# Kernel optimization log

Hardware: AMD Instinct MI355X
Metric: run time of the kernel (lower is better)

The kernel has to match this reference:

```python
import jax, jax.numpy as jnp
import numpy as np

EMBED = 768
HEADS = 12
HEAD_DIM = EMBED // HEADS
DEPTH = 4
PATCH = 16
GRID = 32  # 512 / 16
MLP_DIM = 4 * EMBED
LN_EPS = 1e-5


def layer_norm(x, w, b):
    m = jnp.mean(x, axis=-1, keepdims=True)
    v = jnp.mean(jnp.square(x - m), axis=-1, keepdims=True)
    return (x - m) * jax.lax.rsqrt(v + LN_EPS) * w + b


def sam_attention(x, qkv_w, qkv_b, proj_w, proj_b, rel_pos_h, rel_pos_w):
    B, H, W, C = x.shape
    N = H * W
    scale = HEAD_DIM ** -0.5
    qkv = x.reshape(B, N, C) @ qkv_w + qkv_b  # (B, N, 3C)
    qkv = qkv.reshape(B, N, 3, HEADS, HEAD_DIM).transpose(2, 0, 3, 1, 4)
    qkv = qkv.reshape(3, B * HEADS, N, HEAD_DIM)
    q, k, v = qkv[0], qkv[1], qkv[2]
    attn = jnp.einsum('bqc,bkc->bqk', q * scale, k)  # (B*nh, N, N)
    # decomposed relative position (q_size == k_size, table already max_rel_dist)
    idx_h = jnp.arange(H)[:, None] - jnp.arange(H)[None, :] + (H - 1)
    idx_w = jnp.arange(W)[:, None] - jnp.arange(W)[None, :] + (W - 1)
    Rh = rel_pos_h[idx_h]  # (H, H, hd)
    Rw = rel_pos_w[idx_w]  # (W, W, hd)
    r_q = q.reshape(B * HEADS, H, W, HEAD_DIM)
    rel_h = jnp.einsum('bhwc,hkc->bhwk', r_q, Rh)
    rel_w = jnp.einsum('bhwc,wkc->bhwk', r_q, Rw)
    attn = (attn.reshape(B * HEADS, H, W, H, W)
            + rel_h[:, :, :, :, None]
            + rel_w[:, :, :, None, :]).reshape(B * HEADS, N, N)
    attn = jax.nn.softmax(attn, axis=-1)
    out = (attn @ v).reshape(B, HEADS, H, W, HEAD_DIM)
    out = out.transpose(0, 2, 3, 1, 4).reshape(B, H, W, C)
    return out @ proj_w + proj_b


def setup_inputs() -> dict:
    key = jax.random.key(0)
    ks = jax.random.split(key, 20)
    s = lambda k, shape, sc=0.02: jax.random.normal(k, shape, jnp.float32) * sc
    inp = {
        'x': jax.random.normal(ks[0], (4, 3, 512, 512), jnp.float32),
        'conv_w': s(ks[1], (EMBED, 3, PATCH, PATCH)),
        'conv_b': jnp.zeros((EMBED,), jnp.float32),
        'pos_embed': s(ks[2], (1, GRID, GRID, EMBED)),
        'ln1_w': jnp.ones((DEPTH, EMBED), jnp.float32),
        'ln1_b': jnp.zeros((DEPTH, EMBED), jnp.float32),
        'qkv_w': s(ks[3], (DEPTH, EMBED, 3 * EMBED)),
        'qkv_b': jnp.zeros((DEPTH, 3 * EMBED), jnp.float32),
        'proj_w': s(ks[4], (DEPTH, EMBED, EMBED)),
        'proj_b': jnp.zeros((DEPTH, EMBED), jnp.float32),
        'rel_pos_h': s(ks[5], (DEPTH, 2 * GRID - 1, HEAD_DIM)),
        'rel_pos_w': s(ks[6], (DEPTH, 2 * GRID - 1, HEAD_DIM)),
        'ln2_w': jnp.ones((DEPTH, EMBED), jnp.float32),
        'ln2_b': jnp.zeros((DEPTH, EMBED), jnp.float32),
        'fc1_w': s(ks[7], (DEPTH, EMBED, MLP_DIM)),
        'fc1_b': jnp.zeros((DEPTH, MLP_DIM), jnp.float32),
        'fc2_w': s(ks[8], (DEPTH, MLP_DIM, EMBED)),
        'fc2_b': jnp.zeros((DEPTH, EMBED), jnp.float32),
    }
    return inp


def reference(x, conv_w, conv_b, pos_embed, ln1_w, ln1_b, qkv_w, qkv_b,
              proj_w, proj_b, rel_pos_h, rel_pos_w, ln2_w, ln2_b,
              fc1_w, fc1_b, fc2_w, fc2_b):
    # patch embed: conv stride=patch, then NCHW -> NHWC
    h = jax.lax.conv_general_dilated(
        x, conv_w, window_strides=(PATCH, PATCH), padding='VALID',
        dimension_numbers=('NCHW', 'OIHW', 'NCHW'))
    h = h.transpose(0, 2, 3, 1) + conv_b  # (B, 32, 32, 768)
    h = h + pos_embed
    for i in range(DEPTH):
        a = sam_attention(layer_norm(h, ln1_w[i], ln1_b[i]),
                          qkv_w[i], qkv_b[i], proj_w[i], proj_b[i],
                          rel_pos_h[i], rel_pos_w[i])
        h = h + a
        m = layer_norm(h, ln2_w[i], ln2_b[i])
        m = jax.nn.gelu(m @ fc1_w[i] + fc1_b[i], approximate=False) @ fc2_w[i] + fc2_b[i]
        h = h + m
    return h
```

## Files before the change

kernel.cpp:

```cpp
#include <hip/hip_runtime.h>
#include <hip/hip_bf16.h>
#include <math.h>
#include <stdint.h>

#define EMBED 768
#define NTOK  1024
#define BATCH 4
#define NHEAD 12
#define HD    64
#define MLPD  3072
#define M_ROWS 4096

typedef __attribute__((ext_vector_type(8))) short short8;
typedef __attribute__((ext_vector_type(4))) float floatx4;

__device__ __forceinline__ float b2f(__hip_bfloat16 v) { return __bfloat162float(v); }

__device__ __forceinline__ void gld_lds16(const void* g, void* l) {
    __builtin_amdgcn_global_load_lds(
        (const __attribute__((address_space(1))) uint32_t*)g,
        (__attribute__((address_space(3))) uint32_t*)l, 16, 0, 0);
}

__device__ __forceinline__ int swz(int row, int c) { return row*64 + (((c) ^ (row & 7)) << 3); }

__device__ __forceinline__ void xcd_remap(int gx, int gy, int& bx, int& by) {
    int id  = blockIdx.x + gx*blockIdx.y;
    int nwg = gx*gy;
    int q = nwg >> 3, r = nwg & 7;
    int xcd = id & 7, idx = id >> 3;
    int nid = (xcd < r ? xcd*(q+1) : r*(q+1) + (xcd-r)*q) + idx;
    bx = nid % gx;
    by = nid / gx;
}

__global__ __launch_bounds__(256)
void im2col(const float* __restrict__ x, __hip_bfloat16* __restrict__ A)
{
    int p  = blockIdx.x;
    int b  = p >> 10;
    int n  = p & 1023;
    int gh = n >> 5, gw = n & 31;
    int tid = threadIdx.x;
    for (int i = tid; i < 768; i += 256) {
        int ci = i >> 8, r = i & 255, kh = r >> 4, kw = r & 15;
        A[(size_t)p*768 + i] = __float2bfloat16(
            x[(((size_t)b*3 + ci)*512 + (gh*16 + kh))*512 + gw*16 + kw]);
    }
}

__global__ __launch_bounds__(256)
void cvt_bf16(const float* __restrict__ in, __hip_bfloat16* __restrict__ out, int n)
{
    int i = blockIdx.x*256 + threadIdx.x;
    if (i < n) out[i] = __float2bfloat16(in[i]);
}

__global__ __launch_bounds__(256)
void layernorm_bf16(const float* __restrict__ in,
                    const float* __restrict__ w,
                    const float* __restrict__ b,
                    __hip_bfloat16* __restrict__ out)
{
    int row = blockIdx.x;
    const float* xr = in + (size_t)row*768;
    int tid = threadIdx.x;
    float v0 = xr[tid], v1 = xr[tid+256], v2 = xr[tid+512];
    float s = v0+v1+v2, ss = v0*v0+v1*v1+v2*v2;
    __shared__ float rs[256], rss[256];
    rs[tid] = s; rss[tid] = ss; __syncthreads();
    for (int o = 128; o > 0; o >>= 1) {
        if (tid < o) { rs[tid] += rs[tid+o]; rss[tid] += rss[tid+o]; }
        __syncthreads();
    }
    float mean = rs[0] * (1.f/768.f);
    float var  = rss[0] * (1.f/768.f) - mean*mean;
    float inv  = rsqrtf(var + 1e-5f);
    out[(size_t)row*768 + tid]     = __float2bfloat16((v0-mean)*inv*w[tid]     + b[tid]);
    out[(size_t)row*768 + tid+256] = __float2bfloat16((v1-mean)*inv*w[tid+256] + b[tid+256]);
    out[(size_t)row*768 + tid+512] = __float2bfloat16((v2-mean)*inv*w[tid+512] + b[tid+512]);
}

__global__ __launch_bounds__(256)
void resum_ln(float* __restrict__ h,
              const float* __restrict__ p0, const float* __restrict__ p1,
              const float* __restrict__ bias,
              const float* __restrict__ w, const float* __restrict__ b,
              __hip_bfloat16* __restrict__ out)
{
    int row = blockIdx.x;
    int tid = threadIdx.x;
    size_t base = (size_t)row*768;
    float v[3];
    float s = 0.f, ss = 0.f;
    #pragma unroll
    for (int e = 0; e < 3; ++e) {
        int i = tid + e*256;
        float val = h[base+i] + p0[base+i] + p1[base+i] + bias[i];
        h[base+i] = val;
        v[e] = val; s += val; ss += val*val;
    }
    __shared__ float rs[256], rss[256];
    rs[tid] = s; rss[tid] = ss; __syncthreads();
    for (int o = 128; o > 0; o >>= 1) {
        if (tid < o) { rs[tid] += rs[tid+o]; rss[tid] += rss[tid+o]; }
        __syncthreads();
    }
    float mean = rs[0] * (1.f/768.f);
    float var  = rss[0] * (1.f/768.f) - mean*mean;
    float inv  = rsqrtf(var + 1e-5f);
    #pragma unroll
    for (int e = 0; e < 3; ++e) {
        int i = tid + e*256;
        out[base+i] = __float2bfloat16((v[e]-mean)*inv*w[i] + b[i]);
    }
}

__global__ __launch_bounds__(256)
void resum_out(const float* __restrict__ h,
               const float* __restrict__ p0, const float* __restrict__ p1,
               const float* __restrict__ bias,
               float* __restrict__ out)
{
    int i = blockIdx.x*256 + threadIdx.x;
    out[i] = h[i] + p0[i] + p1[i] + bias[i % 768];
}

__global__ __launch_bounds__(256)
void prep_weights(const float* __restrict__ qkv_w,  const float* __restrict__ proj_w,
                  const float* __restrict__ fc1_w,  const float* __restrict__ fc2_w,
                  __hip_bfloat16* __restrict__ qkv_wt, __hip_bfloat16* __restrict__ proj_wt,
                  __hip_bfloat16* __restrict__ fc1_wt, __hip_bfloat16* __restrict__ fc2_wt)
{
    int id = blockIdx.x;
    const float* src; __hip_bfloat16* dst; int K, N, bx, by;
    if (id < 1728)      {            src = qkv_w;  dst = qkv_wt;  K = 768;  N = 2304; bx = id % 72; by = id / 72; }
    else if (id < 2304) { id -= 1728; src = proj_w; dst = proj_wt; K = 768;  N = 768;  bx = id % 24; by = id / 24; }
    else if (id < 4608) { id -= 2304; src = fc1_w;  dst = fc1_wt;  K = 768;  N = 3072; bx = id % 96; by = id / 96; }
    else                { id -= 4608; src = fc2_w;  dst = fc2_wt;  K = 3072; N = 768;  bx = id % 24; by = id / 24; }

    __shared__ float t[32][33];
    int n0 = bx*32, k0 = by*32;
    int tx = threadIdx.x & 31, ty = threadIdx.x >> 5;
    #pragma unroll
    for (int r = 0; r < 4; ++r) {
        int row = ty + r*8;
        t[row][tx] = src[(size_t)(k0+row)*N + n0 + tx];
    }
    __syncthreads();
    #pragma unroll
    for (int r = 0; r < 4; ++r) {
        int row = ty + r*8;
        dst[(size_t)(n0+row)*K + k0 + tx] = __float2bfloat16(t[tx][row]);
    }
}

__global__ __launch_bounds__(256)
void gemm64(const __hip_bfloat16* __restrict__ A,
            const __hip_bfloat16* __restrict__ Bt,
            const float* __restrict__ bias,
            const float* __restrict__ res,
            const float* __restrict__ posadd,
            float* __restrict__ Cf,
            int M, int N, int K)
{
    __shared__ __align__(16) char smem[24576];

    const int tid  = threadIdx.x;
    const int lane = tid & 63;
    const int wid  = tid >> 6;
    const int wr   = wid >> 1;
    const int wc   = wid & 1;
    const int lr   = lane & 15;
    const int quad = lane >> 4;

    int bx, by;
    xcd_remap(gridDim.x, gridDim.y, bx, by);
    const int bm = by * 64;
    const int bn = bx * 128;

    const int srow  = tid >> 2;
    const int skoff = (tid & 3) * 8;
    const int wbase = wid * 1024;

    floatx4 acc[2][4];
    #pragma unroll
    for (int i = 0; i < 2; ++i)
        #pragma unroll
        for (int j = 0; j < 4; ++j)
            acc[i][j] = (floatx4){0.f,0.f,0.f,0.f};

    auto stage = [&](int bq, int k0) {
        char* base = smem + bq*12288 + wbase;
        gld_lds16(A + (size_t)(bm + srow)*K + k0 + skoff, base);
        #pragma unroll
        for (int c = 0; c < 2; ++c)
            gld_lds16(Bt + (size_t)(bn + c*64 + srow)*K + k0 + skoff,
                      base + 4096 + c*4096);
    };

    const int nt = K >> 5;
    stage(0, 0);
    __syncthreads();
    int cur = 0;
    for (int t = 0; t < nt; ++t) {
        if (t + 1 < nt) stage(cur ^ 1, (t+1)*32);

        const __hip_bfloat16* As = (const __hip_bfloat16*)(smem + cur*12288);
        const __hip_bfloat16* Bs = As + 2048;

        short8 a[2], b[4];
        #pragma unroll
        for (int i = 0; i < 2; ++i)
            a[i] = *(const short8*)((const void*)(As + (wr*32 + i*16 + lr)*32 + quad*8));
        #pragma unroll
        for (int j = 0; j < 4; ++j)
            b[j] = *(const short8*)((const void*)(Bs + (wc*64 + j*16 + lr)*32 + quad*8));
        #pragma unroll
        for (int i = 0; i < 2; ++i)
            #pragma unroll
            for (int j = 0; j < 4; ++j)
                acc[i][j] = __builtin_amdgcn_mfma_f32_16x16x32_bf16(a[i], b[j], acc[i][j], 0, 0, 0);
        __syncthreads();
        cur ^= 1;
    }

    #pragma unroll
    for (int j = 0; j < 4; ++j) {
        int col = bn + wc*64 + j*16 + lr;
        float bs = bias[col];
        #pragma unroll
        for (int i = 0; i < 2; ++i) {
            #pragma unroll
            for (int r = 0; r < 4; ++r) {
                int row = bm + wr*32 + i*16 + quad*4 + r;
                float val = acc[i][j][r] + bs;
                if (res)    val += res[(size_t)row*N + col];
                if (posadd) val += posadd[(size_t)(row & 1023)*N + col];
                Cf[(size_t)row*N + col] = val;
            }
        }
    }
}

__global__ __launch_bounds__(256)
void gemm128(const __hip_bfloat16* __restrict__ A,
             const __hip_bfloat16* __restrict__ Bt,
             const float* __restrict__ bias,
             float* __restrict__ Cf,
             __hip_bfloat16* __restrict__ Cb,
             __hip_bfloat16* __restrict__ qp,
             __hip_bfloat16* __restrict__ kp,
             __hip_bfloat16* __restrict__ vp,
             int M, int N, int K, int S, int dogelu, int emode)
{
    __shared__ __align__(16) char smem[32768];

    const int tid  = threadIdx.x;
    const int lane = tid & 63;
    const int wid  = tid >> 6;
    const int wr   = wid >> 1;
    const int wc   = wid & 1;
    const int lr   = lane & 15;
    const int quad = lane >> 4;

    int bx, by;
    xcd_remap(gridDim.x, gridDim.y, bx, by);
    const int bm = by * 128;
    const int bn = bx * 128;
    const int z  = blockIdx.z;
    const int Kseg = K / S;
    const int kbeg = z * Kseg;

    const int srow  = tid >> 2;
    const int skoff = (tid & 3) * 8;
    const int wbase = wid * 1024;

    floatx4 acc[4][4];
    #pragma unroll
    for (int i = 0; i < 4; ++i)
        #pragma unroll
        for (int j = 0; j < 4; ++j)
            acc[i][j] = (floatx4){0.f,0.f,0.f,0.f};

    auto stage = [&](int bq, int k0) {
        char* base = smem + bq*16384 + wbase;
        #pragma unroll
        for (int c = 0; c < 2; ++c)
            gld_lds16(A + (size_t)(bm + c*64 + srow)*K + k0 + skoff,
                      base + c*4096);
        #pragma unroll
        for (int c = 0; c < 2; ++c)
            gld_lds16(Bt + (size_t)(bn + c*64 + srow)*K + k0 + skoff,
                      base + 8192 + c*4096);
    };

    const int nt = Kseg >> 5;
    stage(0, kbeg);
    __syncthreads();
    int cur = 0;
    for (int t = 0; t < nt; ++t) {
        if (t + 1 < nt) stage(cur ^ 1, kbeg + (t+1)*32);

        const __hip_bfloat16* As = (const __hip_bfloat16*)(smem + cur*16384);
        const __hip_bfloat16* Bs = As + 4096;

        short8 a[4], b[4];
        #pragma unroll
        for (int i = 0; i < 4; ++i)
            a[i] = *(const short8*)((const void*)(As + (wr*64 + i*16 + lr)*32 + quad*8));
        #pragma unroll
        for (int j = 0; j < 4; ++j)
            b[j] = *(const short8*)((const void*)(Bs + (wc*64 + j*16 + lr)*32 + quad*8));
        #pragma unroll
        for (int i = 0; i < 4; ++i)
            #pragma unroll
            for (int j = 0; j < 4; ++j)
                acc[i][j] = __builtin_amdgcn_mfma_f32_16x16x32_bf16(a[i], b[j], acc[i][j], 0, 0, 0);
        __syncthreads();
        cur ^= 1;
    }

    if (emode == 3) {
        #pragma unroll
        for (int j = 0; j < 4; ++j) {
            int col = bn + wc*64 + j*16 + lr;
            #pragma unroll
            for (int i = 0; i < 4; ++i) {
                #pragma unroll
                for (int r = 0; r < 4; ++r) {
                    int row = bm + wr*64 + i*16 + quad*4 + r;
                    Cf[(size_t)z*M*N + (size_t)row*N + col] = acc[i][j][r];
                }
            }
        }
        return;
    }

    __hip_bfloat16* epi = (__hip_bfloat16*)(smem + wid*4864);

    if (emode == 1) {
        #pragma unroll
        for (int p = 0; p < 2; ++p) {
            #pragma unroll
            for (int j = 0; j < 4; ++j) {
                float bs = bias[bn + wc*64 + j*16 + lr];
                #pragma unroll
                for (int ii = 0; ii < 2; ++ii) {
                    int i = p*2 + ii;
                    #pragma unroll
                    for (int r = 0; r < 4; ++r) {
                        float val = acc[i][j][r] + bs;
                        if (dogelu) val = 0.5f*val*(1.f + erff(val*0.70710678118f));
                        epi[(ii*16 + quad*4 + r)*72 + j*16 + lr] = __float2bfloat16(val);
                    }
                }
            }
            #pragma unroll
            for (int p2 = 0; p2 < 4; ++p2) {
                int row = p2*8 + (lane >> 3), chunk = lane & 7;
                short8 v = *(const short8*)((const void*)(epi + row*72 + chunk*8));
                *(short8*)((void*)(Cb + (size_t)(bm + wr*64 + p*32 + row)*N
                                      + bn + wc*64 + chunk*8)) = v;
            }
        }
        return;
    }

    const int head64 = (bn + wc*64) >> 6;
    const int which  = head64 / 12;
    const int head   = head64 % 12;
    const int b_     = (bm + wr*64) >> 10;
    const int bh     = b_*NHEAD + head;
    const int n0     = (bm + wr*64) & 1023;

    if (which < 2) {
        __hip_bfloat16* dst = (which == 0 ? qp : kp) + ((size_t)bh*NTOK + n0)*HD;
        #pragma unroll
        for (int p = 0; p < 2; ++p) {
            #pragma unroll
            for (int j = 0; j < 4; ++j) {
                float bs = bias[bn + wc*64 + j*16 + lr];
                #pragma unroll
                for (int ii = 0; ii < 2; ++ii) {
                    int i = p*2 + ii;
                    #pragma unroll
                    for (int r = 0; r < 4; ++r)
                        epi[(ii*16 + quad*4 + r)*72 + j*16 + lr] =
                            __float2bfloat16(acc[i][j][r] + bs);
                }
            }
            #pragma unroll
            for (int p2 = 0; p2 < 4; ++p2) {
                int row = p2*8 + (lane >> 3), chunk = lane & 7;
                short8 v = *(const short8*)((const void*)(epi + row*72 + chunk*8));
                *(short8*)((void*)(dst + (size_t)(p*32 + row)*HD + chunk*8)) = v;
            }
        }
    } else {
        __hip_bfloat16* dstv = vp + (size_t)bh*HD*NTOK + n0;
        #pragma unroll
        for (int p = 0; p < 2; ++p) {
            #pragma unroll
            for (int j = 0; j < 4; ++j) {
                float bs = bias[bn + wc*64 + j*16 + lr];
                #pragma unroll
                for (int ii = 0; ii < 2; ++ii) {
                    int i = p*2 + ii;
                    #pragma unroll
                    for (int r = 0; r < 4; ++r)
                        epi[(j*16 + lr)*36 + ii*16 + quad*4 + r] =
                            __float2bfloat16(acc[i][j][r] + bs);
                }
            }
            #pragma unroll
            for (int p2 = 0; p2 < 4; ++p2) {
                int d = p2*16 + (lane >> 2), chunk = lane & 3;
                short8 v = *(const short8*)((const void*)(epi + d*36 + chunk*8));
                *(short8*)((void*)(dstv + (size_t)d*NTOK + p*32 + chunk*8)) = v;
            }
        }
    }
}

__global__ __launch_bounds__(256)
void attention_mfma(const __hip_bfloat16* __restrict__ qp,
                    const __hip_bfloat16* __restrict__ kp,
                    const __hip_bfloat16* __restrict__ vp,
                    const float* __restrict__ rph,
                    const float* __restrict__ rpw,
                    __hip_bfloat16* __restrict__ out)
{
    const int blk  = blockIdx.x;
    const int bh   = blk >> 4;
    const int qt   = blk & 15;
    const int b    = bh / NHEAD;
    const int head = bh % NHEAD;
    const int tid  = threadIdx.x;
    const int lane = tid & 63;
    const int w    = tid >> 6;
    const int lr   = lane & 15;
    const int quad = lane >> 4;

    __shared__ __align__(16) __hip_bfloat16 Qs[64*64];
    __shared__ __align__(16) __hip_bfloat16 Ks[64*64];
    __shared__ __align__(16) __hip_bfloat16 Vs[64*64];
    __shared__ __align__(16) __hip_bfloat16 Ps[4*16*64];
    __shared__ float relhS[64*32];
    __shared__ float relwS[64*32];

    const __hip_bfloat16* qb = qp + ((size_t)bh*NTOK + qt*64)*HD;
    const __hip_bfloat16* kb = kp + (size_t)bh*NTOK*HD;
    const __hip_bfloat16* vb = vp + (size_t)bh*HD*NTOK;

    const int sr = tid >> 2;
    const int sc = (tid & 3) * 2;

    short8 kreg0, kreg1, vreg0, vreg1;
    {
        const __hip_bfloat16* kk = kb + (size_t)sr*HD + sc*8;
        kreg0 = *(const short8*)((const void*)kk);
        kreg1 = *(const short8*)((const void*)(kk + 8));
        const __hip_bfloat16* vv = vb + (size_t)sr*NTOK + sc*8;
        vreg0 = *(const short8*)((const void*)vv);
        vreg1 = *(const short8*)((const void*)(vv + 8));
    }

    {
        const __hip_bfloat16* qq = qb + (size_t)sr*HD + sc*8;
        short8 q0 = *(const short8*)((const void*)qq);
        short8 q1 = *(const short8*)((const void*)(qq + 8));
        *(short8*)((void*)(Qs + swz(sr, sc)))   = q0;
        *(short8*)((void*)(Qs + swz(sr, sc+1))) = q1;
    }

    for (int i = tid; i < 504; i += 256) {
        int r = i >> 3, c = i & 7;
        const float* ph = rph + (size_t)r*HD + c*8;
        const float* pw = rpw + (size_t)r*HD + c*8;
        union { short8 v; __hip_bfloat16 e[8]; } uh, uw;
        #pragma unroll
        for (int e = 0; e < 8; ++e) { uh.e[e] = __float2bfloat16(ph[e]); uw.e[e] = __float2bfloat16(pw[e]); }
        *(short8*)((void*)(Ks + swz(r, c))) = uh.v;
        *(short8*)((void*)(Vs + swz(r, c))) = uw.v;
    }
    if (tid < 16) {
        short8 z = (short8){0,0,0,0,0,0,0,0};
        int c = tid & 7;
        if (tid < 8) *(short8*)((void*)(Ks + swz(63, c))) = z;
        else         *(short8*)((void*)(Vs + swz(63, c))) = z;
    }
    __syncthreads();

    short8 qa0 = *(const short8*)((const void*)(Qs + swz(w*16 + lr, quad)));
    short8 qa1 = *(const short8*)((const void*)(Qs + swz(w*16 + lr, 4 + quad)));

    const int qrow = w*16 + quad*4;
    const int qh_  = qt*2 + (w >> 1);
    const int qw_  = (w & 1)*16 + quad*4;

    #pragma unroll
    for (int j = 0; j < 4; ++j) {
        int t = j*16 + lr;
        short8 th0 = *(const short8*)((const void*)(Ks + swz(j*16 + lr, quad)));
        short8 th1 = *(const short8*)((const void*)(Ks + swz(j*16 + lr, 4 + quad)));
        floatx4 ha = (floatx4){0.f,0.f,0.f,0.f};
        ha = __builtin_amdgcn_mfma_f32_16x16x32_bf16(qa0, th0, ha, 0, 0, 0);
        ha = __builtin_amdgcn_mfma_f32_16x16x32_bf16(qa1, th1, ha, 0, 0, 0);
        short8 tw0 = *(const short8*)((const void*)(Vs + swz(j*16 + lr, quad)));
        short8 tw1 = *(const short8*)((const void*)(Vs + swz(j*16 + lr, 4 + quad)));
        floatx4 wa = (floatx4){0.f,0.f,0.f,0.f};
        wa = __builtin_amdgcn_mfma_f32_16x16x32_bf16(qa0, tw0, wa, 0, 0, 0);
        wa = __builtin_amdgcn_mfma_f32_16x16x32_bf16(qa1, tw1, wa, 0, 0, 0);
        int kh = qh_ + 31 - t;
        #pragma unroll
        for (int rr = 0; rr < 4; ++rr) {
            if (kh >= 0 && kh < 32) relhS[(qrow + rr)*32 + kh] = ha[rr];
            int kw = qw_ + rr + 31 - t;
            if (kw >= 0 && kw < 32) relwS[(qrow + rr)*32 + kw] = wa[rr];
        }
    }

    float rw[4][2];
    #pragma unroll
    for (int rr = 0; rr < 4; ++rr)
        #pragma unroll
        for (int jp = 0; jp < 2; ++jp)
            rw[rr][jp] = relwS[(qrow + rr)*32 + jp*16 + lr];

    floatx4 o[4];
    #pragma unroll
    for (int ds = 0; ds < 4; ++ds) o[ds] = (floatx4){0.f,0.f,0.f,0.f};
    float lsum[4] = {0.f, 0.f, 0.f, 0.f};

    const float scale = 0.125f;

    for (int kt = 0; kt < 16; ++kt) {
        __syncthreads();
        *(short8*)((void*)(Ks + swz(sr, sc)))   = kreg0;
        *(short8*)((void*)(Ks + swz(sr, sc+1))) = kreg1;
        *(short8*)((void*)(Vs + swz(sr, sc)))   = vreg0;
        *(short8*)((void*)(Vs + swz(sr, sc+1))) = vreg1;
        __syncthreads();

        if (kt < 15) {
            const __hip_bfloat16* kk = kb + (size_t)(kt+1)*64*HD + (size_t)sr*HD + sc*8;
            kreg0 = *(const short8*)((const void*)kk);
            kreg1 = *(const short8*)((const void*)(kk + 8));
            const __hip_bfloat16* vv = vb + (size_t)sr*NTOK + (kt+1)*64 + sc*8;
            vreg0 = *(const short8*)((const void*)vv);
            vreg1 = *(const short8*)((const void*)(vv + 8));
        }

        float2 rh2[4];
        #pragma unroll
        for (int rr = 0; rr < 4; ++rr)
            rh2[rr] = *(const float2*)((const void*)(relhS + (qrow + rr)*32 + kt*2));

        floatx4 sv[4];
        #pragma unroll
        for (int j = 0; j < 4; ++j) {
            short8 kb0 = *(const short8*)((const void*)(Ks + swz(j*16 + lr, quad)));
            short8 kb1 = *(const short8*)((const void*)(Ks + swz(j*16 + lr, 4 + quad)));
            floatx4 z = (floatx4){0.f,0.f,0.f,0.f};
            z = __builtin_amdgcn_mfma_f32_16x16x32_bf16(qa0, kb0, z, 0, 0, 0);
            z = __builtin_amdgcn_mfma_f32_16x16x32_bf16(qa1, kb1, z, 0, 0, 0);
            sv[j] = z;
        }

        #pragma unroll
        for (int j = 0; j < 4; ++j) {
            int colc = j*2 + (lr >> 3);
            #pragma unroll
            for (int rr = 0; rr < 4; ++rr) {
                float s = sv[j][rr]*scale + ((j < 2) ? rh2[rr].x : rh2[rr].y) + rw[rr][j & 1];
                s = fminf(fmaxf(s, -60.f), 60.f);
                float pp = __expf(s);
                lsum[rr] += pp;
                int prow = quad*4 + rr;
                Ps[w*1024 + prow*64 + ((colc ^ (prow & 7)) << 3) + (lr & 7)] = __float2bfloat16(pp);
            }
        }

        short8 pa0 = *(const short8*)((const void*)(Ps + w*1024 + swz(lr, quad)));
        short8 pa1 = *(const short8*)((const void*)(Ps + w*1024 + swz(lr, 4 + quad)));
        #pragma unroll
        for (int ds = 0; ds < 4; ++ds) {
            short8 v0 = *(const short8*)((const void*)(Vs + swz(ds*16 + lr, quad)));
            short8 v1 = *(const short8*)((const void*)(Vs + swz(ds*16 + lr, 4 + quad)));
            o[ds] = __builtin_amdgcn_mfma_f32_16x16x32_bf16(pa0, v0, o[ds], 0, 0, 0);
            o[ds] = __builtin_amdgcn_mfma_f32_16x16x32_bf16(pa1, v1, o[ds], 0, 0, 0);
        }
    }

    #pragma unroll
    for (int off = 1; off < 16; off <<= 1)
        #pragma unroll
        for (int rr = 0; rr < 4; ++rr)
            lsum[rr] += __shfl_xor(lsum[rr], off, 16);

    #pragma unroll
    for (int rr = 0; rr < 4; ++rr) {
        float inv = 1.f / lsum[rr];
        int n = qt*64 + w*16 + quad*4 + rr;
        size_t base = ((size_t)b*NTOK + n)*EMBED + head*HD;
        #pragma unroll
        for (int ds = 0; ds < 4; ++ds)
            out[base + ds*16 + lr] = __float2bfloat16(o[ds][rr] * inv);
    }
}

extern "C" void kernel_launch(void* const* d_in, const int* in_sizes, int n_in,
                              void* d_out, int out_size, void* d_ws, size_t ws_size,
                              hipStream_t stream)
{
    const float* x      = (const float*)d_in[0];
    const float* conv_w = (const float*)d_in[1];
    const float* conv_b = (const float*)d_in[2];
    const float* pos    = (const float*)d_in[3];
    const float* ln1_w  = (const float*)d_in[4];
    const float* ln1_b  = (const float*)d_in[5];
    const float* qkv_w  = (const float*)d_in[6];
    const float* qkv_b  = (const float*)d_in[7];
    const float* proj_w = (const float*)d_in[8];
    const float* proj_b = (const float*)d_in[9];
    const float* rph    = (const float*)d_in[10];
    const float* rpw    = (const float*)d_in[11];
    const float* ln2_w  = (const float*)d_in[12];
    const float* ln2_b  = (const float*)d_in[13];
    const float* fc1_w  = (const float*)d_in[14];
    const float* fc1_b  = (const float*)d_in[15];
    const float* fc2_w  = (const float*)d_in[16];
    const float* fc2_b  = (const float*)d_in[17];

    char* p = (char*)d_ws;
    float*           h       = (float*)p;           p += (size_t)M_ROWS*EMBED*4;
    __hip_bfloat16*  q_perm  = (__hip_bfloat16*)p;
    float*           p0      = (float*)p;           p += (size_t)48*NTOK*HD*2;
    __hip_bfloat16*  k_perm  = (__hip_bfloat16*)p;  p += (size_t)48*NTOK*HD*2;
    __hip_bfloat16*  vt_perm = (__hip_bfloat16*)p;  p += (size_t)48*NTOK*HD*2;
    __hip_bfloat16*  attn_o  = (__hip_bfloat16*)p;  p += (size_t)M_ROWS*EMBED*2;
    __hip_bfloat16*  x_ln    = (__hip_bfloat16*)p;  p += (size_t)M_ROWS*EMBED*2;
    __hip_bfloat16*  mlp     = (__hip_bfloat16*)p;  p += (size_t)M_ROWS*MLPD*2;
    __hip_bfloat16*  qkv_wt  = (__hip_bfloat16*)p;  p += (size_t)2304*768*2;
    __hip_bfloat16*  proj_wt = (__hip_bfloat16*)p;  p += (size_t)768*768*2;
    __hip_bfloat16*  fc1_wt  = (__hip_bfloat16*)p;  p += (size_t)MLPD*768*2;
    __hip_bfloat16*  fc2_wt  = (__hip_bfloat16*)p;  p += (size_t)768*MLPD*2;

    __hip_bfloat16*  A_im    = mlp;
    __hip_bfloat16*  conv_wt = qkv_wt;

    im2col<<<M_ROWS, 256, 0, stream>>>(x, A_im);
    cvt_bf16<<<(768*768 + 255)/256, 256, 0, stream>>>(conv_w, conv_wt, 768*768);
    gemm64<<<dim3(768/128, M_ROWS/64, 1), 256, 0, stream>>>(
        A_im, conv_wt, conv_b, nullptr, pos, h, M_ROWS, 768, 768);

    layernorm_bf16<<<M_ROWS, 256, 0, stream>>>(h, ln1_w, ln1_b, x_ln);

    for (int L = 0; L < 4; ++L) {
        prep_weights<<<6912, 256, 0, stream>>>(
            qkv_w + (size_t)L*768*2304, proj_w + (size_t)L*768*768,
            fc1_w + (size_t)L*768*MLPD, fc2_w + (size_t)L*MLPD*768,
            qkv_wt, proj_wt, fc1_wt, fc2_wt);

        gemm128<<<dim3(2304/128, M_ROWS/128, 1), 256, 0, stream>>>(
            x_ln, qkv_wt, qkv_b + (size_t)L*3*EMBED,
            nullptr, nullptr, q_perm, k_perm, vt_perm,
            M_ROWS, 2304, 768, 1, 0, 2);

        attention_mfma<<<48*16, 256, 0, stream>>>(
            q_perm, k_perm, vt_perm,
            rph + (size_t)L*63*64, rpw + (size_t)L*63*64, attn_o);

        gemm64<<<dim3(768/128, M_ROWS/64, 1), 256, 0, stream>>>(
            attn_o, proj_wt, proj_b + (size_t)L*EMBED, h, nullptr,
            h, M_ROWS, 768, 768);

        layernorm_bf16<<<M_ROWS, 256, 0, stream>>>(h, ln2_w + L*EMBED, ln2_b + L*EMBED, x_ln);

        gemm128<<<dim3(MLPD/128, M_ROWS/128, 1), 256, 0, stream>>>(
            x_ln, fc1_wt, fc1_b + (size_t)L*MLPD,
            nullptr, mlp, nullptr, nullptr, nullptr,
            M_ROWS, MLPD, 768, 1, 1, 1);

        gemm128<<<dim3(768/128, M_ROWS/128, 2), 256, 0, stream>>>(
            mlp, fc2_wt, nullptr,
            p0, nullptr, nullptr, nullptr, nullptr,
            M_ROWS, 768, MLPD, 2, 0, 3);

        float* p1 = p0 + (size_t)M_ROWS*768;
        if (L < 3) {
            resum_ln<<<M_ROWS, 256, 0, stream>>>(
                h, p0, p1, fc2_b + (size_t)L*EMBED,
                ln1_w + (size_t)(L+1)*EMBED, ln1_b + (size_t)(L+1)*EMBED, x_ln);
        } else {
            resum_out<<<M_ROWS*EMBED/256, 256, 0, stream>>>(
                h, p0, p1, fc2_b + (size_t)L*EMBED, (float*)d_out);
        }
    }
}
```

Before: 960.2 us.

## Swizzle GEMM LDS layout and restructure double-buffer pipeline with explicit waitcnts

Both GEMM kernels now XOR-swizzle the k-chunk offset when staging global-to-LDS loads and apply the matching swizzle on the fragment reads, to reduce LDS bank conflicts. The prologue issues two stages up front. The loop waits on vmcnt and a raw s_barrier, reads fragments, waits on lgkmcnt, barriers again, then issues the load two tiles ahead into the buffer just consumed, so loads overlap the MFMAs. This relies on hand-counted vmcnt values matching the number of outstanding loads per thread. Any mismatch or compiler reordering would cause races.

```diff
diff --git a/kernel.cpp b/kernel.cpp
--- a/kernel.cpp
+++ b/kernel.cpp
@@ -180,8 +180,8 @@
     const int bn = bx * 128;
 
     const int srow  = tid >> 2;
-    const int skoff = (tid & 3) * 8;
-    const int wbase = wid * 1024;
+    const int skoff = ((tid & 3) ^ ((tid >> 3) & 3)) * 8;
+    const int csw   = (quad ^ ((lr >> 1) & 3)) * 8;
 
     floatx4 acc[2][4];
     #pragma unroll
@@ -191,7 +191,7 @@
             acc[i][j] = (floatx4){0.f,0.f,0.f,0.f};
 
     auto stage = [&](int bq, int k0) {
-        char* base = smem + bq*12288 + wbase;
+        char* base = smem + bq*12288 + (wid * 1024);
         gld_lds16(A + (size_t)(bm + srow)*K + k0 + skoff, base);
         #pragma unroll
         for (int c = 0; c < 2; ++c)
@@ -201,10 +201,12 @@
 
     const int nt = K >> 5;
     stage(0, 0);
-    __syncthreads();
+    stage(1, 32);
     int cur = 0;
     for (int t = 0; t < nt; ++t) {
-        if (t + 1 < nt) stage(cur ^ 1, (t+1)*32);
+        if (t + 1 < nt) asm volatile("s_waitcnt vmcnt(3)" ::: "memory");
+        else            asm volatile("s_waitcnt vmcnt(0)" ::: "memory");
+        __builtin_amdgcn_s_barrier();
 
         const __hip_bfloat16* As = (const __hip_bfloat16*)(smem + cur*12288);
         const __hip_bfloat16* Bs = As + 2048;
@@ -212,16 +214,21 @@
         short8 a[2], b[4];
         #pragma unroll
         for (int i = 0; i < 2; ++i)
-            a[i] = *(const short8*)((const void*)(As + (wr*32 + i*16 + lr)*32 + quad*8));
+            a[i] = *(const short8*)((const void*)(As + (wr*32 + i*16 + lr)*32 + csw));
         #pragma unroll
         for (int j = 0; j < 4; ++j)
-            b[j] = *(const short8*)((const void*)(Bs + (wc*64 + j*16 + lr)*32 + quad*8));
+            b[j] = *(const short8*)((const void*)(Bs + (wc*64 + j*16 + lr)*32 + csw));
+        asm volatile("s_waitcnt lgkmcnt(0)" ::: "memory");
+        __builtin_amdgcn_sched_barrier(0);
+        __builtin_amdgcn_s_barrier();
+
+        if (t + 2 < nt) stage(cur, (t+2)*32);
+
         #pragma unroll
         for (int i = 0; i < 2; ++i)
             #pragma unroll
             for (int j = 0; j < 4; ++j)
                 acc[i][j] = __builtin_amdgcn_mfma_f32_16x16x32_bf16(a[i], b[j], acc[i][j], 0, 0, 0);
-        __syncthreads();
         cur ^= 1;
     }
 
@@ -273,8 +280,8 @@
     const int kbeg = z * Kseg;
 
     const int srow  = tid >> 2;
-    const int skoff = (tid & 3) * 8;
-    const int wbase = wid * 1024;
+    const int skoff = ((tid & 3) ^ ((tid >> 3) & 3)) * 8;
+    const int csw   = (quad ^ ((lr >> 1) & 3)) * 8;
 
     floatx4 acc[4][4];
     #pragma unroll
@@ -284,7 +291,7 @@
             acc[i][j] = (floatx4){0.f,0.f,0.f,0.f};
 
     auto stage = [&](int bq, int k0) {
-        char* base = smem + bq*16384 + wbase;
+        char* base = smem + bq*16384 + (wid * 1024);
         #pragma unroll
         for (int c = 0; c < 2; ++c)
             gld_lds16(A + (size_t)(bm + c*64 + srow)*K + k0 + skoff,
@@ -297,10 +304,12 @@
 
     const int nt = Kseg >> 5;
     stage(0, kbeg);
-    __syncthreads();
+    stage(1, kbeg + 32);
     int cur = 0;
     for (int t = 0; t < nt; ++t) {
-        if (t + 1 < nt) stage(cur ^ 1, kbeg + (t+1)*32);
+        if (t + 1 < nt) asm volatile("s_waitcnt vmcnt(4)" ::: "memory");
+        else            asm volatile("s_waitcnt vmcnt(0)" ::: "memory");
+        __builtin_amdgcn_s_barrier();
 
         const __hip_bfloat16* As = (const __hip_bfloat16*)(smem + cur*16384);
         const __hip_bfloat16* Bs = As + 4096;
@@ -308,16 +317,21 @@
         short8 a[4], b[4];
         #pragma unroll
         for (int i = 0; i < 4; ++i)
-            a[i] = *(const short8*)((const void*)(As + (wr*64 + i*16 + lr)*32 + quad*8));
+            a[i] = *(const short8*)((const void*)(As + (wr*64 + i*16 + lr)*32 + csw));
         #pragma unroll
         for (int j = 0; j < 4; ++j)
-            b[j] = *(const short8*)((const void*)(Bs + (wc*64 + j*16 + lr)*32 + quad*8));
+            b[j] = *(const short8*)((const void*)(Bs + (wc*64 + j*16 + lr)*32 + csw));
+        asm volatile("s_waitcnt lgkmcnt(0)" ::: "memory");
+        __builtin_amdgcn_sched_barrier(0);
+        __builtin_amdgcn_s_barrier();
+
+        if (t + 2 < nt) stage(cur, kbeg + (t+2)*32);
+
         #pragma unroll
         for (int i = 0; i < 4; ++i)
             #pragma unroll
             for (int j = 0; j < 4; ++j)
                 acc[i][j] = __builtin_amdgcn_mfma_f32_16x16x32_bf16(a[i], b[j], acc[i][j], 0, 0, 0);
-        __syncthreads();
         cur ^= 1;
     }
 
```

After: 898.0 us. 1.07x faster.
